# Optimization experiments

Hardware: AMD Instinct MI355X
Metric: run time of the kernel (lower is better)

## Reference

```python
import jax, jax.numpy as jnp
import numpy as np

N = 50000      # nodes
E = 800000     # edges (avg degree 16)
F_IN = 128     # input feature dim
HID = 64       # hidden_channels
HEADS = 4
OUT = 64       # out_channels


def _gatv2_layer(x, src, dst, Wl, Wr, att, bias, heads, ch, n):
    # lin_l (source) and lin_r (target) projections -> [N, H, C]
    xl = (x @ Wl).reshape(n, heads, ch)
    xr = (x @ Wr).reshape(n, heads, ch)
    # per-edge GATv2 attention logits: a^T LeakyReLU(xl_j + xr_i)
    e = jax.nn.leaky_relu(xl[src] + xr[dst], negative_slope=0.2)  # [E, H, C]
    score = jnp.einsum('ehc,hc->eh', e, att)                      # [E, H]
    # segment softmax over incoming edges of each destination node
    m = jax.ops.segment_max(score, dst, num_segments=n)           # [N, H]
    m = jnp.where(jnp.isfinite(m), m, 0.0)
    p = jnp.exp(score - m[dst])
    denom = jax.ops.segment_sum(p, dst, num_segments=n)           # [N, H]
    alpha = p / (denom[dst] + 1e-16)                              # [E, H]
    # weighted scatter-aggregate of source messages xl_j
    out = jax.ops.segment_sum(alpha[..., None] * xl[src], dst, num_segments=n)
    return out.reshape(n, heads * ch) + bias


def setup_inputs() -> dict:
    key = jax.random.key(0)
    ks = jax.random.split(key, 16)

    def w(k, shape, fan_in):
        return (jax.random.normal(k, shape, dtype=jnp.float32) / np.sqrt(fan_in)).astype(jnp.float32)

    return {
        'x': jax.random.normal(ks[0], (N, F_IN), dtype=jnp.float32),
        'Wl1': w(ks[1], (F_IN, HEADS * HID), F_IN),
        'Wr1': w(ks[2], (F_IN, HEADS * HID), F_IN),
        'att1': w(ks[3], (HEADS, HID), HID),
        'b1': jnp.zeros((HEADS * HID,), jnp.float32),
        'Wl2': w(ks[4], (HEADS * HID, HEADS * HID), HEADS * HID),
        'Wr2': w(ks[5], (HEADS * HID, HEADS * HID), HEADS * HID),
        'att2': w(ks[6], (HEADS, HID), HID),
        'b2': jnp.zeros((HEADS * HID,), jnp.float32),
        'Wl3': w(ks[7], (HEADS * HID, OUT), HEADS * HID),
        'Wr3': w(ks[8], (HEADS * HID, OUT), HEADS * HID),
        'att3': w(ks[9], (1, OUT), OUT),
        'b3': jnp.zeros((OUT,), jnp.float32),
        'Wlin': w(ks[10], (OUT, HID), OUT),
        'blin': jnp.zeros((HID,), jnp.float32),
        'edge_index': jax.random.randint(ks[11], (2, E), 0, N, dtype=jnp.int64
                                         if jax.config.read('jax_enable_x64') else jnp.int32),
    }


def reference(x, Wl1, Wr1, att1, b1, Wl2, Wr2, att2, b2, Wl3, Wr3, att3, b3, Wlin, blin, edge_index):
    src, dst = edge_index[0], edge_index[1]
    h = jax.nn.elu(_gatv2_layer(x, src, dst, Wl1, Wr1, att1, b1, HEADS, HID, N))
    h = jax.nn.elu(_gatv2_layer(h, src, dst, Wl2, Wr2, att2, b2, HEADS, HID, N))
    h = _gatv2_layer(h, src, dst, Wl3, Wr3, att3, b3, 1, OUT, N)
    # F.dropout(p=0.5, training=False) -> identity in eval mode
    return h @ Wlin + blin
```

## Files before the change

kernel.cpp:

```cpp
#include <hip/hip_runtime.h>
#include <hip/hip_fp16.h>

#define NN 50000
#define EE 800000

typedef float f32x4 __attribute__((ext_vector_type(4)));
typedef _Float16 f16x8 __attribute__((ext_vector_type(8)));
typedef _Float16 f16x4 __attribute__((ext_vector_type(4)));
typedef _Float16 f16x2 __attribute__((ext_vector_type(2)));

__global__ void hist_kernel(const int* __restrict__ dst, int* __restrict__ counts, int E) {
    int idx = blockIdx.x * blockDim.x + threadIdx.x;
    int stride = gridDim.x * blockDim.x;
    for (int e = idx; e < E; e += stride)
        atomicAdd(&counts[dst[e]], 1);
}

__global__ void scan_phaseA(const int* __restrict__ counts, int* __restrict__ bsum, int n) {
    __shared__ int buf[256];
    int b = blockIdx.x, t = threadIdx.x;
    int i = b * 256 + t;
    buf[t] = (i < n) ? counts[i] : 0;
    __syncthreads();
#pragma unroll
    for (int off = 128; off; off >>= 1) {
        if (t < off) buf[t] += buf[t + off];
        __syncthreads();
    }
    if (t == 0) bsum[b] = buf[0];
}

__global__ void scan_phaseB(int* __restrict__ bsum, int* __restrict__ row_off_n, int nb) {
    __shared__ int buf[256];
    int t = threadIdx.x;
    int v = (t < nb) ? bsum[t] : 0;
    buf[t] = v;
    __syncthreads();
#pragma unroll
    for (int off = 1; off < 256; off <<= 1) {
        int x = (t >= off) ? buf[t - off] : 0;
        __syncthreads();
        buf[t] += x;
        __syncthreads();
    }
    if (t < nb) bsum[t] = buf[t] - v;
    if (t == 255) *row_off_n = buf[255];
}

__global__ void scan_phaseC(const int* __restrict__ counts, const int* __restrict__ bsum,
                            int* __restrict__ row_off, int n) {
    __shared__ int buf[256];
    int b = blockIdx.x, t = threadIdx.x;
    int i = b * 256 + t;
    int v = (i < n) ? counts[i] : 0;
    buf[t] = v;
    __syncthreads();
#pragma unroll
    for (int off = 1; off < 256; off <<= 1) {
        int x = (t >= off) ? buf[t - off] : 0;
        __syncthreads();
        buf[t] += x;
        __syncthreads();
    }
    if (i < n) row_off[i] = bsum[b] + buf[t] - v;
}

__global__ void scatter_kernel(const int* __restrict__ src, const int* __restrict__ dst,
                               const int* __restrict__ row_off, int* __restrict__ cursor,
                               int* __restrict__ esrc, int E) {
    int idx = blockIdx.x * blockDim.x + threadIdx.x;
    int stride = gridDim.x * blockDim.x;
    for (int e = idx; e < E; e += stride) {
        int d = dst[e];
        int pos = row_off[d] + atomicAdd(&cursor[d], 1);
        esrc[pos] = src[e];
    }
}

__device__ __forceinline__ void wfrag_store(__half* o, int K, int col, int k, float v) {
    int KS = K >> 5;
    int cgni = col >> 4, l15 = col & 15;
    int ks = k >> 5, qq = (k >> 3) & 3, ee = k & 7;
    size_t flat = ((size_t)(cgni * KS + ks) * 64 + qq * 16 + l15) * 8 + ee;
    o[flat] = __float2half_rn(v);
}

__global__ void prep_all(const float* __restrict__ Wl1, const float* __restrict__ Wr1,
                         const float* __restrict__ Wl2, const float* __restrict__ Wr2,
                         const float* __restrict__ Wl3, const float* __restrict__ Wr3,
                         const float* __restrict__ Wlin,
                         __half* __restrict__ w1, __half* __restrict__ w2,
                         __half* __restrict__ w3, __half* __restrict__ w4,
                         const float* __restrict__ x, __half* __restrict__ xf, int n4x) {
    int idx = blockIdx.x * blockDim.x + threadIdx.x;
    if (idx < 233472) {
        const float* W; __half* o; int K, Nc, roff, li;
        if (idx < 65536) {
            K = 128; Nc = 256; o = w1;
            if (idx < 32768) { W = Wl1; li = idx; roff = 0; }
            else             { W = Wr1; li = idx - 32768; roff = 256; }
        } else if (idx < 196608) {
            K = 256; Nc = 256; o = w2;
            if (idx < 131072) { W = Wl2; li = idx - 65536; roff = 0; }
            else              { W = Wr2; li = idx - 131072; roff = 256; }
        } else if (idx < 229376) {
            K = 256; Nc = 64; o = w3;
            if (idx < 212992) { W = Wl3; li = idx - 196608; roff = 0; }
            else              { W = Wr3; li = idx - 212992; roff = 64; }
        } else {
            K = 64; Nc = 64; o = w4; W = Wlin; li = idx - 229376; roff = 0;
        }
        int k = li / Nc, n = li - k * Nc;
        wfrag_store(o, K, roff + n, k, W[li]);
    } else {
        int xi = idx - 233472;
        if (xi < n4x) {
            float4 v = *(const float4*)(x + (size_t)xi * 4);
            f16x4 h = {(_Float16)v.x, (_Float16)v.y, (_Float16)v.z, (_Float16)v.w};
            *(f16x4*)((_Float16*)xf + (size_t)xi * 4) = h;
        }
    }
}

template <int KS, int COLG>
__global__ __launch_bounds__(COLG * 256) void gemm_ws(
        const __half* __restrict__ A, const __half* __restrict__ Bt,
        int M, int nTiles, int Nc, int splitCol,
        __half* __restrict__ outL, __half* __restrict__ outR,
        float* __restrict__ outF, const float* __restrict__ bias) {
    constexpr int K = KS * 32;
    int tid = threadIdx.x;
    int lane = tid & 63;
    int w = tid >> 6;
    int rs = w & 3;
    int cg = w >> 2;
    int l15 = lane & 15, q = lane >> 4;
    int colbase = blockIdx.y * (COLG * 64) + cg * 64;

    const _Float16* Ap = (const _Float16*)A;
    const f16x8* Bf = (const f16x8*)Bt;
    int cgni0 = (blockIdx.y * COLG + cg) * 4;

    f16x8 bfrag[KS][4];
#pragma unroll
    for (int ks = 0; ks < KS; ++ks)
#pragma unroll
        for (int ni = 0; ni < 4; ++ni)
            bfrag[ks][ni] = Bf[((size_t)(cgni0 + ni) * KS + ks) * 64 + lane];

    int tile = blockIdx.x;
    if (tile >= nTiles) return;

    f16x8 afrag[KS];
    {
        int row = tile * 64 + rs * 16 + l15;
        if (row >= M) row = M - 1;
        const _Float16* ap = Ap + (size_t)row * K + q * 8;
#pragma unroll
        for (int ks = 0; ks < KS; ++ks) afrag[ks] = *(const f16x8*)(ap + ks * 32);
    }

    while (true) {
        int next = tile + gridDim.x;
        bool has = (next < nTiles);
        f16x8 anext[KS];
        if (has) {
            int row = next * 64 + rs * 16 + l15;
            if (row >= M) row = M - 1;
            const _Float16* ap = Ap + (size_t)row * K + q * 8;
#pragma unroll
            for (int ks = 0; ks < KS; ++ks) anext[ks] = *(const f16x8*)(ap + ks * 32);
        }

        f32x4 acc[4] = {};
#pragma unroll
        for (int ks = 0; ks < KS; ++ks)
#pragma unroll
            for (int ni = 0; ni < 4; ++ni)
                acc[ni] = __builtin_amdgcn_mfma_f32_16x16x32_f16(afrag[ks], bfrag[ks][ni], acc[ni], 0, 0, 0);

#pragma unroll
        for (int ni = 0; ni < 4; ++ni) {
            int gc = colbase + ni * 16 + l15;
            if (outF) {
                float bv = bias ? bias[gc] : 0.f;
#pragma unroll
                for (int r = 0; r < 4; ++r) {
                    int gr = tile * 64 + rs * 16 + q * 4 + r;
                    if (gr < M) outF[(size_t)gr * Nc + gc] = acc[ni][r] + bv;
                }
            } else {
                __half* dp = outL; int cc = gc;
                if (gc >= splitCol) { dp = outR; cc = gc - splitCol; }
#pragma unroll
                for (int r = 0; r < 4; ++r) {
                    int gr = tile * 64 + rs * 16 + q * 4 + r;
                    if (gr < M) dp[(size_t)gr * splitCol + cc] = __float2half_rn(acc[ni][r]);
                }
            }
        }
        if (!has) break;
#pragma unroll
        for (int ks = 0; ks < KS; ++ks) afrag[ks] = anext[ks];
        tile = next;
    }
}

__global__ __launch_bounds__(256) void gat_gather_h4(
        const __half* __restrict__ xl, const __half* __restrict__ xr,
        const float* __restrict__ att, const float* __restrict__ bias,
        const int* __restrict__ row_off, const int* __restrict__ esrc,
        __half* __restrict__ out, int n) {
    const float LOG2E = 1.44269504f;
    int wave = threadIdx.x >> 6;
    int lane = threadIdx.x & 63;
    int node = blockIdx.x * 4 + wave;
    if (node >= n) return;
    int half = lane >> 5;
    unsigned j = lane & 31;

    const uint4* xl4 = (const uint4*)xl;
    uint4 xraw = ((const uint4*)xr)[((unsigned)node << 5) + j];
    f16x2 xrv[4] = {*(const f16x2*)&xraw.x, *(const f16x2*)&xraw.y,
                    *(const f16x2*)&xraw.z, *(const f16x2*)&xraw.w};
    float4 aA = *(const float4*)(att + j * 8);
    float4 aB = *(const float4*)(att + j * 8 + 4);
    f16x2 atv[4] = {{(_Float16)(aA.x * LOG2E), (_Float16)(aA.y * LOG2E)},
                    {(_Float16)(aA.z * LOG2E), (_Float16)(aA.w * LOG2E)},
                    {(_Float16)(aB.x * LOG2E), (_Float16)(aB.y * LOG2E)},
                    {(_Float16)(aB.z * LOG2E), (_Float16)(aB.w * LOG2E)}};
    const f16x2 k02 = {(_Float16)0.2f, (_Float16)0.2f};

    float acc0[8] = {}, acc1[8] = {};
    float l0 = 0.f, l1 = 0.f;

    int e0 = row_off[node], e1 = row_off[node + 1];
    int elast = e1 - 1;

#define H4_BODY(EBASE, ACC, LSUM)                                             \
    {                                                                         \
        int idx_ = EBASE + half;                                              \
        int s_ = esrc[min(idx_, elast)];                                      \
        uint4 raw_ = xl4[((unsigned)s_ << 5) + j];                            \
        f16x2 v0_ = *(const f16x2*)&raw_.x;                                   \
        f16x2 v1_ = *(const f16x2*)&raw_.y;                                   \
        f16x2 v2_ = *(const f16x2*)&raw_.z;                                   \
        f16x2 v3_ = *(const f16x2*)&raw_.w;                                   \
        f16x2 s0_ = v0_ + xrv[0], s1_ = v1_ + xrv[1];                         \
        f16x2 s2_ = v2_ + xrv[2], s3_ = v3_ + xrv[3];                         \
        f16x2 r0_ = __builtin_elementwise_max(s0_, s0_ * k02);                \
        f16x2 r1_ = __builtin_elementwise_max(s1_, s1_ * k02);                \
        f16x2 r2_ = __builtin_elementwise_max(s2_, s2_ * k02);                \
        f16x2 r3_ = __builtin_elementwise_max(s3_, s3_ * k02);                \
        float t_ = __builtin_amdgcn_fdot2(r0_, atv[0], 0.f, false);           \
        t_ = __builtin_amdgcn_fdot2(r1_, atv[1], t_, false);                  \
        t_ = __builtin_amdgcn_fdot2(r2_, atv[2], t_, false);                  \
        t_ = __builtin_amdgcn_fdot2(r3_, atv[3], t_, false);                  \
        t_ += __shfl_xor(t_, 1);                                              \
        t_ += __shfl_xor(t_, 2);                                              \
        t_ += __shfl_xor(t_, 4);                                              \
        float p_ = exp2f(t_);                                                 \
        p_ = (idx_ < e1) ? p_ : 0.f;                                          \
        LSUM += p_;                                                           \
        ACC[0] = fmaf((float)v0_.x, p_, ACC[0]);                              \
        ACC[1] = fmaf((float)v0_.y, p_, ACC[1]);                              \
        ACC[2] = fmaf((float)v1_.x, p_, ACC[2]);                              \
        ACC[3] = fmaf((float)v1_.y, p_, ACC[3]);                              \
        ACC[4] = fmaf((float)v2_.x, p_, ACC[4]);                              \
        ACC[5] = fmaf((float)v2_.y, p_, ACC[5]);                              \
        ACC[6] = fmaf((float)v3_.x, p_, ACC[6]);                              \
        ACC[7] = fmaf((float)v3_.y, p_, ACC[7]);                              \
    }

    for (int e = e0; e < e1; e += 4) {
        H4_BODY(e, acc0, l0)
        if (e + 2 < e1) H4_BODY(e + 2, acc1, l1)
    }
#undef H4_BODY

    float acc[8];
#pragma unroll
    for (int k = 0; k < 8; ++k) acc[k] = acc0[k] + acc1[k];
    float L = l0 + l1;
#pragma unroll
    for (int k = 0; k < 8; ++k) acc[k] += __shfl_xor(acc[k], 32);
    L += __shfl_xor(L, 32);

    float inv = 1.f / (L + 1e-16f);
    float4 bvA = *(const float4*)(bias + j * 8);
    float4 bvB = *(const float4*)(bias + j * 8 + 4);
    float bb[8] = {bvA.x, bvA.y, bvA.z, bvA.w, bvB.x, bvB.y, bvB.z, bvB.w};
    f16x8 ov;
#pragma unroll
    for (int k = 0; k < 8; ++k) {
        float v = acc[k] * inv + bb[k];
        v = v > 0.f ? v : __expf(v) - 1.f;
        ov[k] = (_Float16)v;
    }
    if (half == 0)
        ((f16x8*)((_Float16*)out + ((size_t)node << 8)))[j] = ov;
}

__global__ __launch_bounds__(256) void gat_gather_h1(
        const __half* __restrict__ xl, const __half* __restrict__ xr,
        const float* __restrict__ att, const float* __restrict__ bias,
        const int* __restrict__ row_off, const int* __restrict__ esrc,
        __half* __restrict__ out, int n) {
    const float LOG2E = 1.44269504f;
    int wave = threadIdx.x >> 6;
    int lane = threadIdx.x & 63;
    int node = blockIdx.x * 4 + wave;
    if (node >= n) return;
    int q4 = lane >> 4;
    unsigned j = lane & 15;

    const uint2* xl2 = (const uint2*)xl;
    uint2 xraw = ((const uint2*)xr)[((unsigned)node << 4) + j];
    f16x2 xrv[2] = {*(const f16x2*)&xraw.x, *(const f16x2*)&xraw.y};
    float4 av = *(const float4*)(att + j * 4);
    f16x2 atv[2] = {{(_Float16)(av.x * LOG2E), (_Float16)(av.y * LOG2E)},
                    {(_Float16)(av.z * LOG2E), (_Float16)(av.w * LOG2E)}};
    const f16x2 k02 = {(_Float16)0.2f, (_Float16)0.2f};

    float acc0[4] = {}, acc1[4] = {};
    float l0 = 0.f, l1 = 0.f;

    int e0 = row_off[node], e1 = row_off[node + 1];
    int elast = e1 - 1;

#define H1_BODY(EBASE, ACC, LSUM)                                             \
    {                                                                         \
        int idx_ = EBASE + q4;                                                \
        int s_ = esrc[min(idx_, elast)];                                      \
        uint2 raw_ = xl2[((unsigned)s_ << 4) + j];                            \
        f16x2 v0_ = *(const f16x2*)&raw_.x;                                   \
        f16x2 v1_ = *(const f16x2*)&raw_.y;                                   \
        f16x2 s0_ = v0_ + xrv[0], s1_ = v1_ + xrv[1];                         \
        f16x2 r0_ = __builtin_elementwise_max(s0_, s0_ * k02);                \
        f16x2 r1_ = __builtin_elementwise_max(s1_, s1_ * k02);                \
        float t_ = __builtin_amdgcn_fdot2(r0_, atv[0], 0.f, false);           \
        t_ = __builtin_amdgcn_fdot2(r1_, atv[1], t_, false);                  \
        t_ += __shfl_xor(t_, 1);                                              \
        t_ += __shfl_xor(t_, 2);                                              \
        t_ += __shfl_xor(t_, 4);                                              \
        t_ += __shfl_xor(t_, 8);                                              \
        float p_ = exp2f(t_);                                                 \
        p_ = (idx_ < e1) ? p_ : 0.f;                                          \
        LSUM += p_;                                                           \
        ACC[0] = fmaf((float)v0_.x, p_, ACC[0]);                              \
        ACC[1] = fmaf((float)v0_.y, p_, ACC[1]);                              \
        ACC[2] = fmaf((float)v1_.x, p_, ACC[2]);                              \
        ACC[3] = fmaf((float)v1_.y, p_, ACC[3]);                              \
    }

    for (int e = e0; e < e1; e += 8) {
        H1_BODY(e, acc0, l0)
        if (e + 4 < e1) H1_BODY(e + 4, acc1, l1)
    }
#undef H1_BODY

    float acc[4];
#pragma unroll
    for (int k = 0; k < 4; ++k) acc[k] = acc0[k] + acc1[k];
    float L = l0 + l1;
#pragma unroll
    for (int k = 0; k < 4; ++k) {
        acc[k] += __shfl_xor(acc[k], 16);
        acc[k] += __shfl_xor(acc[k], 32);
    }
    L += __shfl_xor(L, 16);
    L += __shfl_xor(L, 32);

    float inv = 1.f / (L + 1e-16f);
    float4 bv = *(const float4*)(bias + j * 4);
    f16x4 ov = {(_Float16)(acc[0] * inv + bv.x),
                (_Float16)(acc[1] * inv + bv.y),
                (_Float16)(acc[2] * inv + bv.z),
                (_Float16)(acc[3] * inv + bv.w)};
    if (q4 == 0)
        ((f16x4*)((_Float16*)out + ((size_t)node << 6)))[j] = ov;
}

extern "C" void kernel_launch(void* const* d_in, const int* in_sizes, int n_in,
                              void* d_out, int out_size, void* d_ws, size_t ws_size,
                              hipStream_t stream) {
    const float* x    = (const float*)d_in[0];
    const float* Wl1  = (const float*)d_in[1];
    const float* Wr1  = (const float*)d_in[2];
    const float* att1 = (const float*)d_in[3];
    const float* b1   = (const float*)d_in[4];
    const float* Wl2  = (const float*)d_in[5];
    const float* Wr2  = (const float*)d_in[6];
    const float* att2 = (const float*)d_in[7];
    const float* b2   = (const float*)d_in[8];
    const float* Wl3  = (const float*)d_in[9];
    const float* Wr3  = (const float*)d_in[10];
    const float* att3 = (const float*)d_in[11];
    const float* b3   = (const float*)d_in[12];
    const float* Wlin = (const float*)d_in[13];
    const float* blin = (const float*)d_in[14];
    const int*   ei   = (const int*)d_in[15];
    const int* src = ei;
    const int* dst = ei + EE;

    const int N = NN, E = EE;
    const int NB = (N + 255) / 256;

    __half* xf = (__half*)d_ws;
    __half* xl = xf + (size_t)N * 128;
    __half* xr = xl + (size_t)N * 256;
    __half* H  = xr + (size_t)N * 256;
    __half* G  = H + (size_t)N * 256;
    __half* w1 = G + (size_t)N * 64;
    __half* w2 = w1 + 65536;
    __half* w3 = w2 + 131072;
    __half* w4 = w3 + 32768;
    int* row_off = (int*)(w4 + 4096);
    int* tmp     = row_off + (N + 1);
    int* esrc    = tmp + 2 * N;
    int* bsum    = esrc + E;

    hipMemsetAsync(tmp, 0, (size_t)2 * N * sizeof(int), stream);
    hist_kernel<<<1024, 256, 0, stream>>>(dst, tmp, E);
    scan_phaseA<<<NB, 256, 0, stream>>>(tmp, bsum, N);
    scan_phaseB<<<1, 256, 0, stream>>>(bsum, row_off + N, NB);
    scan_phaseC<<<NB, 256, 0, stream>>>(tmp, bsum, row_off, N);
    scatter_kernel<<<1024, 256, 0, stream>>>(src, dst, row_off, tmp + N, esrc, E);

    int n4x = N * 128 / 4;
    prep_all<<<(233472 + n4x + 255) / 256, 256, 0, stream>>>(
        Wl1, Wr1, Wl2, Wr2, Wl3, Wr3, Wlin, w1, w2, w3, w4, x, xf, n4x);

    int nTiles = (N + 63) / 64;
    int gatherBlocks = (N + 3) / 4;

    gemm_ws<4, 2><<<dim3(128, 4), 512, 0, stream>>>(
        xf, w1, N, nTiles, 512, 256, xl, xr, nullptr, nullptr);
    gat_gather_h4<<<gatherBlocks, 256, 0, stream>>>(xl, xr, att1, b1, row_off, esrc, H, N);

    gemm_ws<8, 2><<<dim3(128, 4), 512, 0, stream>>>(
        H, w2, N, nTiles, 512, 256, xl, xr, nullptr, nullptr);
    gat_gather_h4<<<gatherBlocks, 256, 0, stream>>>(xl, xr, att2, b2, row_off, esrc, H, N);

    gemm_ws<8, 2><<<dim3(256, 1), 512, 0, stream>>>(
        H, w3, N, nTiles, 128, 64, xl, xr, nullptr, nullptr);
    gat_gather_h1<<<gatherBlocks, 256, 0, stream>>>(xl, xr, att3, b3, row_off, esrc, G, N);

    gemm_ws<2, 1><<<dim3(512, 1), 256, 0, stream>>>(
        G, w4, N, nTiles, 64, 64, nullptr, nullptr, (float*)d_out, blin);
}
```

Measured before the change: 486.5 us.

## Widen per-lane features and software-pipeline edge gathers in GAT aggregation kernels

Both gather kernels are restructured so each lane handles twice as many features (16 for 4-head, 8 for 1-head). This lets one wave process 4 or 8 edges at once instead of 2 or 4. The edge loop is software-pipelined: the next edge's source index and feature rows are prefetched a stage ahead. Per-edge score reductions use DPP row operations instead of shuffles, and an occupancy hint is added. The costs are higher register pressure and more cross-slot reduction work at the end.

Measured after the change: 470.2 us. 3.3% less time.

```diff
diff --git a/kernel.cpp b/kernel.cpp
--- a/kernel.cpp
+++ b/kernel.cpp
@@ -206,7 +206,13 @@
     }
 }
 
-__global__ __launch_bounds__(256) void gat_gather_h4(
+template <int CTRL>
+__device__ __forceinline__ float dpp_add_f32(float x) {
+    int y = __builtin_amdgcn_mov_dpp(__float_as_int(x), CTRL, 0xF, 0xF, true);
+    return x + __int_as_float(y);
+}
+
+__global__ __launch_bounds__(256, 6) void gat_gather_h4(
         const __half* __restrict__ xl, const __half* __restrict__ xr,
         const float* __restrict__ att, const float* __restrict__ bias,
         const int* __restrict__ row_off, const int* __restrict__ esrc,
@@ -216,92 +222,108 @@
     int lane = threadIdx.x & 63;
     int node = blockIdx.x * 4 + wave;
     if (node >= n) return;
-    int half = lane >> 5;
-    unsigned j = lane & 31;
-
-    const uint4* xl4 = (const uint4*)xl;
-    uint4 xraw = ((const uint4*)xr)[((unsigned)node << 5) + j];
-    f16x2 xrv[4] = {*(const f16x2*)&xraw.x, *(const f16x2*)&xraw.y,
-                    *(const f16x2*)&xraw.z, *(const f16x2*)&xraw.w};
-    float4 aA = *(const float4*)(att + j * 8);
-    float4 aB = *(const float4*)(att + j * 8 + 4);
-    f16x2 atv[4] = {{(_Float16)(aA.x * LOG2E), (_Float16)(aA.y * LOG2E)},
-                    {(_Float16)(aA.z * LOG2E), (_Float16)(aA.w * LOG2E)},
-                    {(_Float16)(aB.x * LOG2E), (_Float16)(aB.y * LOG2E)},
-                    {(_Float16)(aB.z * LOG2E), (_Float16)(aB.w * LOG2E)}};
+    int eslot = lane >> 4;
+    unsigned j = lane & 15;
+
+    const uint4* xl16 = (const uint4*)xl;
+    unsigned jo = 2u * j;
+
+    f16x2 xrv[8];
+    *(uint4*)(&xrv[0]) = ((const uint4*)xr)[((unsigned)node << 5) + jo];
+    *(uint4*)(&xrv[4]) = ((const uint4*)xr)[((unsigned)node << 5) + jo + 1];
+
+    float4 a0 = *(const float4*)(att + j * 16);
+    float4 a1 = *(const float4*)(att + j * 16 + 4);
+    float4 a2 = *(const float4*)(att + j * 16 + 8);
+    float4 a3 = *(const float4*)(att + j * 16 + 12);
+    f16x2 atv[8] = {
+        {(_Float16)(a0.x * LOG2E), (_Float16)(a0.y * LOG2E)},
+        {(_Float16)(a0.z * LOG2E), (_Float16)(a0.w * LOG2E)},
+        {(_Float16)(a1.x * LOG2E), (_Float16)(a1.y * LOG2E)},
+        {(_Float16)(a1.z * LOG2E), (_Float16)(a1.w * LOG2E)},
+        {(_Float16)(a2.x * LOG2E), (_Float16)(a2.y * LOG2E)},
+        {(_Float16)(a2.z * LOG2E), (_Float16)(a2.w * LOG2E)},
+        {(_Float16)(a3.x * LOG2E), (_Float16)(a3.y * LOG2E)},
+        {(_Float16)(a3.z * LOG2E), (_Float16)(a3.w * LOG2E)}};
     const f16x2 k02 = {(_Float16)0.2f, (_Float16)0.2f};
 
-    float acc0[8] = {}, acc1[8] = {};
-    float l0 = 0.f, l1 = 0.f;
+    float acc[16] = {};
+    float L = 0.f;
 
     int e0 = row_off[node], e1 = row_off[node + 1];
     int elast = e1 - 1;
 
-#define H4_BODY(EBASE, ACC, LSUM)                                             \
-    {                                                                         \
-        int idx_ = EBASE + half;                                              \
-        int s_ = esrc[min(idx_, elast)];                                      \
-        uint4 raw_ = xl4[((unsigned)s_ << 5) + j];                            \
-        f16x2 v0_ = *(const f16x2*)&raw_.x;                                   \
-        f16x2 v1_ = *(const f16x2*)&raw_.y;                                   \
-        f16x2 v2_ = *(const f16x2*)&raw_.z;                                   \
-        f16x2 v3_ = *(const f16x2*)&raw_.w;                                   \
-        f16x2 s0_ = v0_ + xrv[0], s1_ = v1_ + xrv[1];                         \
-        f16x2 s2_ = v2_ + xrv[2], s3_ = v3_ + xrv[3];                         \
-        f16x2 r0_ = __builtin_elementwise_max(s0_, s0_ * k02);                \
-        f16x2 r1_ = __builtin_elementwise_max(s1_, s1_ * k02);                \
-        f16x2 r2_ = __builtin_elementwise_max(s2_, s2_ * k02);                \
-        f16x2 r3_ = __builtin_elementwise_max(s3_, s3_ * k02);                \
-        float t_ = __builtin_amdgcn_fdot2(r0_, atv[0], 0.f, false);           \
-        t_ = __builtin_amdgcn_fdot2(r1_, atv[1], t_, false);                  \
-        t_ = __builtin_amdgcn_fdot2(r2_, atv[2], t_, false);                  \
-        t_ = __builtin_amdgcn_fdot2(r3_, atv[3], t_, false);                  \
-        t_ += __shfl_xor(t_, 1);                                              \
-        t_ += __shfl_xor(t_, 2);                                              \
-        t_ += __shfl_xor(t_, 4);                                              \
-        float p_ = exp2f(t_);                                                 \
-        p_ = (idx_ < e1) ? p_ : 0.f;                                          \
-        LSUM += p_;                                                           \
-        ACC[0] = fmaf((float)v0_.x, p_, ACC[0]);                              \
-        ACC[1] = fmaf((float)v0_.y, p_, ACC[1]);                              \
-        ACC[2] = fmaf((float)v1_.x, p_, ACC[2]);                              \
-        ACC[3] = fmaf((float)v1_.y, p_, ACC[3]);                              \
-        ACC[4] = fmaf((float)v2_.x, p_, ACC[4]);                              \
-        ACC[5] = fmaf((float)v2_.y, p_, ACC[5]);                              \
-        ACC[6] = fmaf((float)v3_.x, p_, ACC[6]);                              \
-        ACC[7] = fmaf((float)v3_.y, p_, ACC[7]);                              \
-    }
+    int sC = esrc[min(e0 + eslot, elast)];
+    int sN = esrc[min(e0 + 4 + eslot, elast)];
+    uint4 g0 = xl16[((unsigned)sC << 5) + jo];
+    uint4 g1 = xl16[((unsigned)sC << 5) + jo + 1];
 
     for (int e = e0; e < e1; e += 4) {
-        H4_BODY(e, acc0, l0)
-        if (e + 2 < e1) H4_BODY(e + 2, acc1, l1)
-    }
-#undef H4_BODY
-
-    float acc[8];
-#pragma unroll
-    for (int k = 0; k < 8; ++k) acc[k] = acc0[k] + acc1[k];
-    float L = l0 + l1;
-#pragma unroll
-    for (int k = 0; k < 8; ++k) acc[k] += __shfl_xor(acc[k], 32);
+        int sF = esrc[min(e + 8 + eslot, elast)];
+        uint4 h0 = xl16[((unsigned)sN << 5) + jo];
+        uint4 h1 = xl16[((unsigned)sN << 5) + jo + 1];
+
+        f16x2 v[8];
+        *(uint4*)(&v[0]) = g0;
+        *(uint4*)(&v[4]) = g1;
+
+        float t0 = 0.f, t1 = 0.f;
+#pragma unroll
+        for (int k = 0; k < 4; ++k) {
+            f16x2 sA = v[k] + xrv[k];
+            f16x2 rA = __builtin_elementwise_max(sA, sA * k02);
+            t0 = __builtin_amdgcn_fdot2(rA, atv[k], t0, false);
+            f16x2 sB = v[k + 4] + xrv[k + 4];
+            f16x2 rB = __builtin_elementwise_max(sB, sB * k02);
+            t1 = __builtin_amdgcn_fdot2(rB, atv[k + 4], t1, false);
+        }
+        float t = t0 + t1;
+        t = dpp_add_f32<0xB1>(t);
+        t = dpp_add_f32<0x4E>(t);
+        float p = exp2f(t);
+        p = (e + eslot < e1) ? p : 0.f;
+        L += p;
+#pragma unroll
+        for (int k = 0; k < 8; ++k) {
+            acc[2 * k]     = fmaf((float)v[k].x, p, acc[2 * k]);
+            acc[2 * k + 1] = fmaf((float)v[k].y, p, acc[2 * k + 1]);
+        }
+        g0 = h0; g1 = h1; sN = sF;
+    }
+
+#pragma unroll
+    for (int k = 0; k < 16; ++k) {
+        acc[k] += __shfl_xor(acc[k], 16);
+        acc[k] += __shfl_xor(acc[k], 32);
+    }
+    L += __shfl_xor(L, 16);
     L += __shfl_xor(L, 32);
 
-    float inv = 1.f / (L + 1e-16f);
-    float4 bvA = *(const float4*)(bias + j * 8);
-    float4 bvB = *(const float4*)(bias + j * 8 + 4);
-    float bb[8] = {bvA.x, bvA.y, bvA.z, bvA.w, bvB.x, bvB.y, bvB.z, bvB.w};
-    f16x8 ov;
-#pragma unroll
-    for (int k = 0; k < 8; ++k) {
-        float v = acc[k] * inv + bb[k];
-        v = v > 0.f ? v : __expf(v) - 1.f;
-        ov[k] = (_Float16)v;
-    }
-    if (half == 0)
-        ((f16x8*)((_Float16*)out + ((size_t)node << 8)))[j] = ov;
-}
-
-__global__ __launch_bounds__(256) void gat_gather_h1(
+    if (eslot == 0) {
+        float inv = 1.f / (L + 1e-16f);
+        float4 b0 = *(const float4*)(bias + j * 16);
+        float4 b1v = *(const float4*)(bias + j * 16 + 4);
+        float4 b2v = *(const float4*)(bias + j * 16 + 8);
+        float4 b3v = *(const float4*)(bias + j * 16 + 12);
+        float bb[16] = {b0.x,  b0.y,  b0.z,  b0.w,  b1v.x, b1v.y, b1v.z, b1v.w,
+                        b2v.x, b2v.y, b2v.z, b2v.w, b3v.x, b3v.y, b3v.z, b3v.w};
+        f16x8 o0, o1;
+#pragma unroll
+        for (int k = 0; k < 8; ++k) {
+            float vA = acc[k] * inv + bb[k];
+            vA = vA > 0.f ? vA : __expf(vA) - 1.f;
+            o0[k] = (_Float16)vA;
+            float vB = acc[k + 8] * inv + bb[k + 8];
+            vB = vB > 0.f ? vB : __expf(vB) - 1.f;
+            o1[k] = (_Float16)vB;
+        }
+        _Float16* op = (_Float16*)out + ((size_t)node << 8) + j * 16;
+        *(f16x8*)op = o0;
+        *(f16x8*)(op + 8) = o1;
+    }
+}
+
+__global__ __launch_bounds__(256, 6) void gat_gather_h1(
         const __half* __restrict__ xl, const __half* __restrict__ xr,
         const float* __restrict__ att, const float* __restrict__ bias,
         const int* __restrict__ row_off, const int* __restrict__ esrc,
@@ -311,74 +333,91 @@
     int lane = threadIdx.x & 63;
     int node = blockIdx.x * 4 + wave;
     if (node >= n) return;
-    int q4 = lane >> 4;
-    unsigned j = lane & 15;
-
-    const uint2* xl2 = (const uint2*)xl;
-    uint2 xraw = ((const uint2*)xr)[((unsigned)node << 4) + j];
-    f16x2 xrv[2] = {*(const f16x2*)&xraw.x, *(const f16x2*)&xraw.y};
-    float4 av = *(const float4*)(att + j * 4);
-    f16x2 atv[2] = {{(_Float16)(av.x * LOG2E), (_Float16)(av.y * LOG2E)},
-                    {(_Float16)(av.z * LOG2E), (_Float16)(av.w * LOG2E)}};
+    int eslot = lane >> 3;
+    unsigned j = lane & 7;
+
+    const uint4* xl16 = (const uint4*)xl;
+
+    f16x2 xrv[4];
+    *(uint4*)(&xrv[0]) = ((const uint4*)xr)[((unsigned)node << 3) + j];
+
+    float4 a0 = *(const float4*)(att + j * 8);
+    float4 a1 = *(const float4*)(att + j * 8 + 4);
+    f16x2 atv[4] = {
+        {(_Float16)(a0.x * LOG2E), (_Float16)(a0.y * LOG2E)},
+        {(_Float16)(a0.z * LOG2E), (_Float16)(a0.w * LOG2E)},
+        {(_Float16)(a1.x * LOG2E), (_Float16)(a1.y * LOG2E)},
+        {(_Float16)(a1.z * LOG2E), (_Float16)(a1.w * LOG2E)}};
     const f16x2 k02 = {(_Float16)0.2f, (_Float16)0.2f};
 
-    float acc0[4] = {}, acc1[4] = {};
-    float l0 = 0.f, l1 = 0.f;
+    float acc[8] = {};
+    float L = 0.f;
 
     int e0 = row_off[node], e1 = row_off[node + 1];
     int elast = e1 - 1;
 
-#define H1_BODY(EBASE, ACC, LSUM)                                             \
-    {                                                                         \
-        int idx_ = EBASE + q4;                                                \
-        int s_ = esrc[min(idx_, elast)];                                      \
-        uint2 raw_ = xl2[((unsigned)s_ << 4) + j];                            \
-        f16x2 v0_ = *(const f16x2*)&raw_.x;                                   \
-        f16x2 v1_ = *(const f16x2*)&raw_.y;                                   \
-        f16x2 s0_ = v0_ + xrv[0], s1_ = v1_ + xrv[1];                         \
-        f16x2 r0_ = __builtin_elementwise_max(s0_, s0_ * k02);                \
-        f16x2 r1_ = __builtin_elementwise_max(s1_, s1_ * k02);                \
-        float t_ = __builtin_amdgcn_fdot2(r0_, atv[0], 0.f, false);           \
-        t_ = __builtin_amdgcn_fdot2(r1_, atv[1], t_, false);                  \
-        t_ += __shfl_xor(t_, 1);                                              \
-        t_ += __shfl_xor(t_, 2);                                              \
-        t_ += __shfl_xor(t_, 4);                                              \
-        t_ += __shfl_xor(t_, 8);                                              \
-        float p_ = exp2f(t_);                                                 \
-        p_ = (idx_ < e1) ? p_ : 0.f;                                          \
-        LSUM += p_;                                                           \
-        ACC[0] = fmaf((float)v0_.x, p_, ACC[0]);                              \
-        ACC[1] = fmaf((float)v0_.y, p_, ACC[1]);                              \
-        ACC[2] = fmaf((float)v1_.x, p_, ACC[2]);                              \
-        ACC[3] = fmaf((float)v1_.y, p_, ACC[3]);                              \
-    }
+    int sC = esrc[min(e0 + eslot, elast)];
+    int sN = esrc[min(e0 + 8 + eslot, elast)];
+    uint4 g = xl16[((unsigned)sC << 3) + j];
 
     for (int e = e0; e < e1; e += 8) {
-        H1_BODY(e, acc0, l0)
-        if (e + 4 < e1) H1_BODY(e + 4, acc1, l1)
-    }
-#undef H1_BODY
-
-    float acc[4];
-#pragma unroll
-    for (int k = 0; k < 4; ++k) acc[k] = acc0[k] + acc1[k];
-    float L = l0 + l1;
-#pragma unroll
-    for (int k = 0; k < 4; ++k) {
+        int sF = esrc[min(e + 16 + eslot, elast)];
+        uint4 h = xl16[((unsigned)sN << 3) + j];
+
+        f16x2 v[4];
+        *(uint4*)(&v[0]) = g;
+
+        float t0 = 0.f, t1 = 0.f;
+        {
+            f16x2 s0 = v[0] + xrv[0];
+            f16x2 r0 = __builtin_elementwise_max(s0, s0 * k02);
+            t0 = __builtin_amdgcn_fdot2(r0, atv[0], t0, false);
+            f16x2 s1 = v[1] + xrv[1];
+            f16x2 r1 = __builtin_elementwise_max(s1, s1 * k02);
+            t0 = __builtin_amdgcn_fdot2(r1, atv[1], t0, false);
+            f16x2 s2 = v[2] + xrv[2];
+            f16x2 r2 = __builtin_elementwise_max(s2, s2 * k02);
+            t1 = __builtin_amdgcn_fdot2(r2, atv[2], t1, false);
+            f16x2 s3 = v[3] + xrv[3];
+            f16x2 r3 = __builtin_elementwise_max(s3, s3 * k02);
+            t1 = __builtin_amdgcn_fdot2(r3, atv[3], t1, false);
+        }
+        float t = t0 + t1;
+        t = dpp_add_f32<0xB1>(t);
+        t = dpp_add_f32<0x4E>(t);
+        t = dpp_add_f32<0x141>(t);
+        float p = exp2f(t);
+        p = (e + eslot < e1) ? p : 0.f;
+        L += p;
+#pragma unroll
+        for (int k = 0; k < 4; ++k) {
+            acc[2 * k]     = fmaf((float)v[k].x, p, acc[2 * k]);
+            acc[2 * k + 1] = fmaf((float)v[k].y, p, acc[2 * k + 1]);
+        }
+        g = h; sN = sF;
+    }
+
+#pragma unroll
+    for (int k = 0; k < 8; ++k) {
+        acc[k] += __shfl_xor(acc[k], 8);
         acc[k] += __shfl_xor(acc[k], 16);
         acc[k] += __shfl_xor(acc[k], 32);
     }
+    L += __shfl_xor(L, 8);
     L += __shfl_xor(L, 16);
     L += __shfl_xor(L, 32);
 
-    float inv = 1.f / (L + 1e-16f);
-    float4 bv = *(const float4*)(bias + j * 4);
-    f16x4 ov = {(_Float16)(acc[0] * inv + bv.x),
-                (_Float16)(acc[1] * inv + bv.y),
-                (_Float16)(acc[2] * inv + bv.z),
-                (_Float16)(acc[3] * inv + bv.w)};
-    if (q4 == 0)
-        ((f16x4*)((_Float16*)out + ((size_t)node << 6)))[j] = ov;
+    if (eslot == 0) {
+        float inv = 1.f / (L + 1e-16f);
+        float4 b0 = *(const float4*)(bias + j * 8);
+        float4 b1v = *(const float4*)(bias + j * 8 + 4);
+        float bb[8] = {b0.x, b0.y, b0.z, b0.w, b1v.x, b1v.y, b1v.z, b1v.w};
+        f16x8 ov;
+#pragma unroll
+        for (int k = 0; k < 8; ++k)
+            ov[k] = (_Float16)(acc[k] * inv + bb[k]);
+        *(f16x8*)((_Float16*)out + ((size_t)node << 6) + j * 8) = ov;
+    }
 }
 
 extern "C" void kernel_launch(void* const* d_in, const int* in_sizes, int n_in,
```
